# Kernel tuning notes

Hardware: AMD Instinct MI355X
Metric: run time of the kernel (lower is better)

## Reference

```python
import jax, jax.numpy as jnp
import numpy as np
from jax import lax

B, CIN, COUT, K, H, W = 16, 512, 512, 3, 64, 64
STYLE_DIM, BASIS, DIRS = 512, 8, 8


def setup_inputs() -> dict:
    key = jax.random.key(0)
    ks = jax.random.split(key, 8)
    return {
        "x": jax.random.normal(ks[0], (B, CIN, H, W), jnp.float32),
        "style": jax.random.normal(ks[1], (B, STYLE_DIM), jnp.float32),
        "weight": jax.random.normal(ks[2], (1, COUT, CIN, K, K), jnp.float32),
        "mod_w": jax.random.normal(ks[3], (CIN, STYLE_DIM), jnp.float32) * 0.02,
        "mod_b": jnp.ones((CIN,), jnp.float32),
        "basis_vectors": jax.random.normal(ks[4], (BASIS, 1, COUT, CIN, K, K), jnp.float32),
        "shifts_coords": jax.random.normal(ks[5], (DIRS, BASIS), jnp.float32),
        "batch_shifts": jax.random.uniform(ks[6], (B,), jnp.float32),
        "batch_directions": jax.random.randint(ks[7], (B,), 0, DIRS),
    }


def reference(x, style, weight, mod_w, mod_b, basis_vectors, shifts_coords,
              batch_shifts, batch_directions):
    batch, in_ch, h, w = x.shape
    out_ch, k = weight.shape[1], weight.shape[3]
    scale = 1.0 / np.sqrt(in_ch * k * k)  # StyleGAN2 equalized-lr scale

    # --- deformation: per-sample weight delta from basis subspace ---
    coefs = shifts_coords[batch_directions]                     # [B, basis]
    bv = basis_vectors.reshape(basis_vectors.shape[0], -1)      # [basis, O*I*k*k]
    delta = coefs @ bv                                          # [B, P]
    nrm = jnp.linalg.norm(delta, axis=1, keepdims=True)
    delta = delta / jnp.maximum(nrm, 1e-12) * batch_shifts[:, None]
    delta = delta.reshape(batch, out_ch, in_ch, k, k)
    wgt = weight + delta                                        # [B, O, I, k, k]

    # --- style modulation + demodulation ---
    s = style @ mod_w.T + mod_b                                 # [B, I]
    wgt = scale * wgt * s[:, None, :, None, None]
    demod = lax.rsqrt(jnp.sum(wgt * wgt, axis=(2, 3, 4)) + 1e-8)  # [B, O]
    wgt = wgt * demod[:, :, None, None, None]

    # --- grouped conv, groups = batch ---
    wgt = wgt.reshape(batch * out_ch, in_ch, k, k)
    xg = x.reshape(1, batch * in_ch, h, w)
    pad = k // 2
    out = lax.conv_general_dilated(
        xg, wgt, window_strides=(1, 1), padding=[(pad, pad), (pad, pad)],
        feature_group_count=batch,
        dimension_numbers=("NCHW", "OIHW", "NCHW"))
    return out.reshape(batch, out_ch, h, w)
```

## Files before the change

kernel.cpp:

```cpp
#include <hip/hip_runtime.h>


typedef __attribute__((ext_vector_type(8))) short bf16x8;
typedef __attribute__((ext_vector_type(4))) float f32x4;

__device__ __forceinline__ unsigned short f2bf(float f) {
  unsigned u = __float_as_uint(f);
  return (unsigned short)((u + 0x7FFFu + ((u >> 16) & 1u)) >> 16);
}

__device__ __forceinline__ void gl_lds16(const void* g, void* l) {
  __builtin_amdgcn_global_load_lds(
      (const __attribute__((address_space(1))) void*)g,
      (__attribute__((address_space(3))) void*)l, 16, 0, 0);
}

template <int N> __device__ __forceinline__ void vm_wait() {
  if constexpr (N == 8) asm volatile("s_waitcnt vmcnt(8)" ::: "memory");
  else if constexpr (N == 0) asm volatile("s_waitcnt vmcnt(0)" ::: "memory");
}

__global__ __launch_bounds__(256) void k_pad(const float* __restrict__ x,
                                             unsigned short* __restrict__ xp) {
  const int bx = blockIdx.x;
  const int b   = bx >> 9;
  const int rem = bx & 511;
  const int y   = rem >> 3;
  const int cb  = rem & 7;
  const int t = threadIdx.x;
  __shared__ float tile[64][65];
  const float* src = x + ((size_t)(b * 512 + cb * 64) * 4096) + y * 64;
#pragma unroll
  for (int r = 0; r < 4; ++r) {
    int idx = r * 256 + t;
    int ch = idx >> 4;
    int xq = (idx & 15) << 2;
    float4 v = *(const float4*)(src + (size_t)ch * 4096 + xq);
    tile[ch][xq + 0] = v.x; tile[ch][xq + 1] = v.y;
    tile[ch][xq + 2] = v.z; tile[ch][xq + 3] = v.w;
  }
  const uint4 z4 = {0u, 0u, 0u, 0u};
  if (t < 16) {
    const int side = t >> 3;
    const int lo = (t & 7) * 8;
    unsigned short* p =
        xp + (((size_t)(b * 66 + y + 1) * 66 + side * 65) * 512 + cb * 64 + lo);
    *(uint4*)p = z4;
  }
  if (y == 0 || y == 63) {
    const int row = (y == 0) ? 0 : 65;
    for (int idx = t; idx < 528; idx += 256) {
      const int c = idx >> 3;
      const int lo = (idx & 7) * 8;
      unsigned short* p =
          xp + (((size_t)(b * 66 + row) * 66 + c) * 512 + cb * 64 + lo);
      *(uint4*)p = z4;
    }
  }
  __syncthreads();
  const int col = t >> 2;
  const int q = t & 3;
  union { unsigned short u16[16]; uint4 v[2]; } pk;
#pragma unroll
  for (int j = 0; j < 16; ++j) pk.u16[j] = f2bf(tile[q * 16 + j][col]);
  unsigned short* dst =
      xp + (((size_t)(b * 66 + y + 1) * 66 + col + 1) * 512 + cb * 64 + q * 16);
  *(uint4*)dst = pk.v[0];
  *(uint4*)(dst + 8) = pk.v[1];
}

__global__ __launch_bounds__(256) void k_mod(const float* __restrict__ style,
                                             const float* __restrict__ mod_w,
                                             const float* __restrict__ mod_b,
                                             float* __restrict__ smod) {
  const int b = blockIdx.x;
  __shared__ float st[512];
  for (int d = threadIdx.x; d < 512; d += 256) st[d] = style[b * 512 + d];
  __syncthreads();
  for (int i = threadIdx.x; i < 512; i += 256) {
    const float* wr = mod_w + (size_t)i * 512;
    float acc = 0.f;
#pragma unroll 4
    for (int d = 0; d < 512; d += 4) {
      float4 wv = *(const float4*)(wr + d);
      acc += wv.x * st[d] + wv.y * st[d + 1] + wv.z * st[d + 2] + wv.w * st[d + 3];
    }
    smod[b * 512 + i] = acc + mod_b[i];
  }
}

__global__ __launch_bounds__(256, 3) void k_gram(const float* __restrict__ bv,
                                                 float* __restrict__ G) {
  const int P4 = 589824;
  float a[36];
#pragma unroll
  for (int c = 0; c < 36; ++c) a[c] = 0.f;
  const float4* bv4 = (const float4*)bv;
  for (int p = blockIdx.x * 256 + threadIdx.x; p < P4; p += gridDim.x * 256) {
    float4 v[8];
#pragma unroll
    for (int k = 0; k < 8; ++k) v[k] = bv4[(size_t)k * P4 + p];
    int c = 0;
#pragma unroll
    for (int i = 0; i < 8; ++i)
#pragma unroll
      for (int j = i; j < 8; ++j) {
        a[c] += v[i].x * v[j].x + v[i].y * v[j].y + v[i].z * v[j].z +
                v[i].w * v[j].w;
        ++c;
      }
  }
#pragma unroll
  for (int c = 0; c < 36; ++c)
#pragma unroll
    for (int off = 32; off > 0; off >>= 1) a[c] += __shfl_down(a[c], off);
  __shared__ float red[4][36];
  const int wv = threadIdx.x >> 6;
  if ((threadIdx.x & 63) == 0)
#pragma unroll
    for (int c = 0; c < 36; ++c) red[wv][c] = a[c];
  __syncthreads();
  if (threadIdx.x < 36)
    atomicAdd(&G[threadIdx.x], red[0][threadIdx.x] + red[1][threadIdx.x] +
                                   red[2][threadIdx.x] + red[3][threadIdx.x]);
}

__global__ void k_amp(const float* __restrict__ shifts_coords,
                      const float* __restrict__ batch_shifts,
                      const int* __restrict__ dirs, const float* __restrict__ G,
                      float* __restrict__ camp) {
  const int b = threadIdx.x;
  if (b < 16) {
    const int dir = dirs[b];
    float c[8];
    for (int k = 0; k < 8; ++k) c[k] = shifts_coords[dir * 8 + k];
    float n2 = 0.f;
    int idx = 0;
    for (int i = 0; i < 8; ++i)
      for (int j = i; j < 8; ++j) {
        float g = G[idx++];
        n2 += (i == j) ? c[i] * c[i] * g : 2.f * c[i] * c[j] * g;
      }
    float nrm = sqrtf(fmaxf(n2, 0.f));
    float amp = batch_shifts[b] / fmaxf(nrm, 1e-12f);
    for (int k = 0; k < 8; ++k) camp[b * 8 + k] = c[k] * amp;
  }
}

__global__ __launch_bounds__(512) void k_weights(const float* __restrict__ weight,
                                                 const float* __restrict__ bv,
                                                 const float* __restrict__ smod,
                                                 const float* __restrict__ camp,
                                                 unsigned short* __restrict__ wgt,
                                                 float* __restrict__ demod) {
  const int o = blockIdx.x;
  const int i = threadIdx.x;
  __shared__ float cl[128];
  __shared__ float red[8][16];
  if (threadIdx.x < 128) cl[threadIdx.x] = camp[threadIdx.x];
  __syncthreads();
  const float scl = 0.014731391274719738f;
  float sm[16];
#pragma unroll
  for (int b = 0; b < 16; ++b) sm[b] = smod[b * 512 + i] * scl;
  float ssq[16];
#pragma unroll
  for (int b = 0; b < 16; ++b) ssq[b] = 0.f;
  const size_t base = ((size_t)o * 512 + i) * 9;
#pragma unroll
  for (int g = 0; g < 3; ++g) {
    float w[3], v[8][3];
#pragma unroll
    for (int q = 0; q < 3; ++q) w[q] = weight[base + g * 3 + q];
#pragma unroll
    for (int k = 0; k < 8; ++k)
#pragma unroll
      for (int q = 0; q < 3; ++q)
        v[k][q] = bv[(size_t)k * 2359296 + base + g * 3 + q];
#pragma unroll
    for (int b = 0; b < 16; ++b) {
#pragma unroll
      for (int q = 0; q < 3; ++q) {
        float d = w[q];
#pragma unroll
        for (int k = 0; k < 8; ++k) d = fmaf(cl[b * 8 + k], v[k][q], d);
        float wv = d * sm[b];
        ssq[b] = fmaf(wv, wv, ssq[b]);
        wgt[(((size_t)(b * 9 + g * 3 + q) * 512 + o) << 9) + i] = f2bf(wv);
      }
    }
  }
#pragma unroll
  for (int b = 0; b < 16; ++b)
#pragma unroll
    for (int off = 32; off > 0; off >>= 1) ssq[b] += __shfl_down(ssq[b], off);
  const int wv_ = threadIdx.x >> 6;
  if ((threadIdx.x & 63) == 0)
#pragma unroll
    for (int b = 0; b < 16; ++b) red[wv_][b] = ssq[b];
  __syncthreads();
  if (threadIdx.x < 16) {
    float s = 0.f;
#pragma unroll
    for (int wq = 0; wq < 8; ++wq) s += red[wq][threadIdx.x];
    demod[threadIdx.x * 512 + o] = rsqrtf(s + 1e-8f);
  }
}

__global__ __launch_bounds__(512, 2) void k_conv(
    const unsigned short* __restrict__ xp, const unsigned short* __restrict__ wgt,
    const float* __restrict__ demod, float* __restrict__ out) {
  extern __shared__ unsigned char smem[];
  const int tid = threadIdx.x;
  const int l = tid & 63;
  const int w = tid >> 6;
  const int wo = w >> 2;
  const int wn = w & 3;

  const int bid = blockIdx.x;
  const int bz = (bid & 7) * 64 + (bid >> 3);
  const int b = bz >> 5;
  const int tt = bz & 31;
  const int o0 = (tt >> 4) << 8;
  const int tn = tt & 15;
  const int n0 = tn << 8;
  const int y0 = tn << 2;

  int swzS[4];
  size_t aByte[4], pBase[4];
#pragma unroll
  for (int r = 0; r < 4; ++r) {
    const int idx = r * 512 + tid;
    const int row = idx >> 3;
    const int swz = ((idx & 7) << 4) ^ ((row & 7) << 4);
    swzS[r] = swz;
    aByte[r] = ((size_t)(o0 + row) << 10) + swz;
    pBase[r] = (size_t)(b * 66 + y0 + (row >> 6)) * 66 + (row & 63);
  }

  const char* wgtc = (const char*)wgt;
  const char* xpc = (const char*)xp;

  auto stage_all = [&](unsigned char* buf, int kt) {
    const int kk = kt >> 3;
    const int is = kt & 7;
    const int ky = kk / 3;
    const int kx = kk - ky * 3;
    const size_t aPlane = ((size_t)(b * 9 + kk) << 19) + ((size_t)is << 7);
    unsigned char* lA = buf;
    unsigned char* lB = buf + 32768;
#pragma unroll
    for (int r = 0; r < 4; ++r)
      gl_lds16(wgtc + aPlane + aByte[r], lA + (r * 512 + tid) * 16);
#pragma unroll
    for (int r = 0; r < 4; ++r)
      gl_lds16(xpc + (((pBase[r] + ky * 66 + kx) << 10) + ((size_t)is << 7) +
                      swzS[r]),
               lB + (r * 512 + tid) * 16);
  };

  f32x4 acc[8][4];
  const f32x4 zz = {0.f, 0.f, 0.f, 0.f};
#pragma unroll
  for (int mi = 0; mi < 8; ++mi)
#pragma unroll
    for (int ni = 0; ni < 4; ++ni) acc[mi][ni] = zz;
  bf16x8 af0[8], af1[8], bf0[4], bf1[4];

  auto rdA = [&](const unsigned char* lA, int MH, bf16x8 (&afx)[8]) {
#pragma unroll
    for (int mi = 0; mi < 4; ++mi)
#pragma unroll
      for (int ks = 0; ks < 2; ++ks) {
        const int row = MH * 128 + wo * 64 + mi * 16 + (l & 15);
        afx[mi * 2 + ks] = *(const bf16x8*)(
            lA + row * 128 + ((ks * 64 + ((l >> 4) << 4)) ^ ((row & 7) << 4)));
      }
  };
  auto rdB = [&](const unsigned char* lB, int NH, bf16x8 (&bfx)[4]) {
#pragma unroll
    for (int ni = 0; ni < 2; ++ni)
#pragma unroll
      for (int ks = 0; ks < 2; ++ks) {
        const int row = NH * 128 + wn * 32 + ni * 16 + (l & 15);
        bfx[ni * 2 + ks] = *(const bf16x8*)(
            lB + row * 128 + ((ks * 64 + ((l >> 4) << 4)) ^ ((row & 7) << 4)));
      }
  };
  auto mma = [&](int MH, int NH, bf16x8 (&afx)[8], bf16x8 (&bfx)[4]) {
    __builtin_amdgcn_s_setprio(1);
#pragma unroll
    for (int mi = 0; mi < 4; ++mi)
#pragma unroll
      for (int ni = 0; ni < 2; ++ni)
#pragma unroll
        for (int ks = 0; ks < 2; ++ks)
          acc[MH * 4 + mi][NH * 2 + ni] =
              __builtin_amdgcn_mfma_f32_16x16x32_bf16(
                  afx[mi * 2 + ks], bfx[ni * 2 + ks],
                  acc[MH * 4 + mi][NH * 2 + ni], 0, 0, 0);
    __builtin_amdgcn_s_setprio(0);
  };

  stage_all(smem, 0);
  stage_all(smem + 65536, 1);
  vm_wait<8>();
  __builtin_amdgcn_s_barrier();

  int cur = 0;
#pragma unroll 1
  for (int kt = 0; kt < 72; ++kt) {
    unsigned char* lA = smem + (cur << 16);
    unsigned char* lB = lA + 32768;
    rdA(lA, 0, af0);
    rdB(lB, 0, bf0);
    rdB(lB, 1, bf1);
    rdA(lA, 1, af1);
    mma(0, 0, af0, bf0);
    mma(0, 1, af0, bf1);
    asm volatile("s_waitcnt lgkmcnt(0)" ::: "memory");
    __builtin_amdgcn_sched_barrier(0);
    __builtin_amdgcn_s_barrier();
    __builtin_amdgcn_sched_barrier(0);
    if (kt < 70) stage_all(lA, kt + 2);
    mma(1, 1, af1, bf1);
    mma(1, 0, af1, bf0);
    if (kt < 70) {
      vm_wait<8>();
      __builtin_amdgcn_s_barrier();
      __builtin_amdgcn_sched_barrier(0);
    } else if (kt == 70) {
      vm_wait<0>();
      __builtin_amdgcn_s_barrier();
      __builtin_amdgcn_sched_barrier(0);
    }
    cur ^= 1;
  }

  float* outb = out + (size_t)(b * 512 + o0) * 4096 + n0;
#pragma unroll
  for (int mh = 0; mh < 2; ++mh)
#pragma unroll
    for (int mi = 0; mi < 4; ++mi) {
      const int orow = mh * 128 + wo * 64 + mi * 16 + ((l >> 4) << 2);
      float dm[4];
#pragma unroll
      for (int r = 0; r < 4; ++r) dm[r] = demod[b * 512 + o0 + orow + r];
#pragma unroll
      for (int nh = 0; nh < 2; ++nh)
#pragma unroll
        for (int ni = 0; ni < 2; ++ni) {
          const int pix = nh * 128 + wn * 32 + ni * 16 + (l & 15);
#pragma unroll
          for (int r = 0; r < 4; ++r)
            outb[(size_t)(orow + r) * 4096 + pix] =
                acc[mh * 4 + mi][nh * 2 + ni][r] * dm[r];
        }
    }
}

extern "C" void kernel_launch(void* const* d_in, const int* in_sizes, int n_in,
                              void* d_out, int out_size, void* d_ws,
                              size_t ws_size, hipStream_t stream) {
  const float* x      = (const float*)d_in[0];
  const float* style  = (const float*)d_in[1];
  const float* weight = (const float*)d_in[2];
  const float* mod_w  = (const float*)d_in[3];
  const float* mod_b  = (const float*)d_in[4];
  const float* bv     = (const float*)d_in[5];
  const float* sc     = (const float*)d_in[6];
  const float* bsh    = (const float*)d_in[7];
  const int*   bdir   = (const int*)d_in[8];
  float* out = (float*)d_out;

  char* ws = (char*)d_ws;
  unsigned short* xp  = (unsigned short*)(ws);
  unsigned short* wgt = (unsigned short*)(ws + 71368704);
  float* G     = (float*)(ws + 146866176);
  float* camp  = (float*)(ws + 146866432);
  float* smod  = (float*)(ws + 146866944);
  float* demod = (float*)(ws + 146899712);

  hipFuncSetAttribute((const void*)k_conv,
                      hipFuncAttributeMaxDynamicSharedMemorySize, 131072);

  hipMemsetAsync(G, 0, 256, stream);
  k_pad<<<8192, 256, 0, stream>>>(x, xp);
  k_mod<<<16, 256, 0, stream>>>(style, mod_w, mod_b, smod);
  k_gram<<<1024, 256, 0, stream>>>(bv, G);
  k_amp<<<1, 64, 0, stream>>>(sc, bsh, bdir, G, camp);
  k_weights<<<512, 512, 0, stream>>>(weight, bv, smod, camp, wgt, demod);
  k_conv<<<512, 512, 131072, stream>>>(xp, wgt, demod, out);
}
```

Before: 418.2 us.

## Use triple-buffered K=32 pipeline with one barrier per step in conv

The conv GEMM main loop moves from a double-buffered K=64 stage with two barriers per step to a triple-buffered K=32 stage (144 steps) with a single barrier each. Each wave now owns a contiguous 128x64 output tile and issues all 32 MFMAs after loading its fragments once, instead of splitting the work into four half-tile phases. The LDS XOR swizzle is dropped for a plain 64-byte row layout, and occupancy hints and dynamic LDS are resized to match. The aim is less barrier stall and better overlap of global-to-LDS loads with compute, at the cost of more loop iterations and possible LDS bank conflicts from the unswizzled reads.

```diff
diff --git a/kernel.cpp b/kernel.cpp
--- a/kernel.cpp
+++ b/kernel.cpp
@@ -16,7 +16,7 @@
 }
 
 template <int N> __device__ __forceinline__ void vm_wait() {
-  if constexpr (N == 8) asm volatile("s_waitcnt vmcnt(8)" ::: "memory");
+  if constexpr (N == 4) asm volatile("s_waitcnt vmcnt(4)" ::: "memory");
   else if constexpr (N == 0) asm volatile("s_waitcnt vmcnt(0)" ::: "memory");
 }
 
@@ -207,7 +207,7 @@
   }
 }
 
-__global__ __launch_bounds__(512, 2) void k_conv(
+__global__ __launch_bounds__(512, 1) void k_conv(
     const unsigned short* __restrict__ xp, const unsigned short* __restrict__ wgt,
     const float* __restrict__ demod, float* __restrict__ out) {
   extern __shared__ unsigned char smem[];
@@ -226,36 +226,36 @@
   const int n0 = tn << 8;
   const int y0 = tn << 2;
 
-  int swzS[4];
-  size_t aByte[4], pBase[4];
-#pragma unroll
-  for (int r = 0; r < 4; ++r) {
+  size_t aOff[2], pBase[2];
+  int sOff[2];
+#pragma unroll
+  for (int r = 0; r < 2; ++r) {
     const int idx = r * 512 + tid;
-    const int row = idx >> 3;
-    const int swz = ((idx & 7) << 4) ^ ((row & 7) << 4);
-    swzS[r] = swz;
-    aByte[r] = ((size_t)(o0 + row) << 10) + swz;
+    const int row = idx >> 2;
+    const int slot = idx & 3;
+    aOff[r] = ((size_t)(o0 + row) << 10) + slot * 16;
     pBase[r] = (size_t)(b * 66 + y0 + (row >> 6)) * 66 + (row & 63);
+    sOff[r] = slot * 16;
   }
 
   const char* wgtc = (const char*)wgt;
   const char* xpc = (const char*)xp;
 
-  auto stage_all = [&](unsigned char* buf, int kt) {
-    const int kk = kt >> 3;
-    const int is = kt & 7;
+  auto stage = [&](unsigned char* buf, int kt) {
+    const int kk = kt >> 4;
+    const int is = kt & 15;
     const int ky = kk / 3;
     const int kx = kk - ky * 3;
-    const size_t aPlane = ((size_t)(b * 9 + kk) << 19) + ((size_t)is << 7);
+    const size_t aPlane = ((size_t)(b * 9 + kk) << 19) + ((size_t)is << 6);
     unsigned char* lA = buf;
-    unsigned char* lB = buf + 32768;
-#pragma unroll
-    for (int r = 0; r < 4; ++r)
-      gl_lds16(wgtc + aPlane + aByte[r], lA + (r * 512 + tid) * 16);
-#pragma unroll
-    for (int r = 0; r < 4; ++r)
-      gl_lds16(xpc + (((pBase[r] + ky * 66 + kx) << 10) + ((size_t)is << 7) +
-                      swzS[r]),
+    unsigned char* lB = buf + 16384;
+#pragma unroll
+    for (int r = 0; r < 2; ++r)
+      gl_lds16(wgtc + aPlane + aOff[r], lA + (r * 512 + tid) * 16);
+#pragma unroll
+    for (int r = 0; r < 2; ++r)
+      gl_lds16(xpc + (((pBase[r] + ky * 66 + kx) << 10) + ((size_t)is << 6) +
+                      sOff[r]),
                lB + (r * 512 + tid) * 16);
   };
 
@@ -265,98 +265,67 @@
   for (int mi = 0; mi < 8; ++mi)
 #pragma unroll
     for (int ni = 0; ni < 4; ++ni) acc[mi][ni] = zz;
-  bf16x8 af0[8], af1[8], bf0[4], bf1[4];
-
-  auto rdA = [&](const unsigned char* lA, int MH, bf16x8 (&afx)[8]) {
-#pragma unroll
-    for (int mi = 0; mi < 4; ++mi)
-#pragma unroll
-      for (int ks = 0; ks < 2; ++ks) {
-        const int row = MH * 128 + wo * 64 + mi * 16 + (l & 15);
-        afx[mi * 2 + ks] = *(const bf16x8*)(
-            lA + row * 128 + ((ks * 64 + ((l >> 4) << 4)) ^ ((row & 7) << 4)));
-      }
-  };
-  auto rdB = [&](const unsigned char* lB, int NH, bf16x8 (&bfx)[4]) {
-#pragma unroll
-    for (int ni = 0; ni < 2; ++ni)
-#pragma unroll
-      for (int ks = 0; ks < 2; ++ks) {
-        const int row = NH * 128 + wn * 32 + ni * 16 + (l & 15);
-        bfx[ni * 2 + ks] = *(const bf16x8*)(
-            lB + row * 128 + ((ks * 64 + ((l >> 4) << 4)) ^ ((row & 7) << 4)));
-      }
-  };
-  auto mma = [&](int MH, int NH, bf16x8 (&afx)[8], bf16x8 (&bfx)[4]) {
+  bf16x8 af[8], bf[4];
+
+  const int rdoff = (l >> 4) << 4;
+
+  unsigned char* p0 = smem;
+  unsigned char* p1 = smem + 32768;
+  unsigned char* p2 = smem + 65536;
+  stage(p0, 0);
+  stage(p1, 1);
+  vm_wait<4>();
+  __builtin_amdgcn_s_barrier();
+  __builtin_amdgcn_sched_barrier(0);
+
+#pragma unroll 1
+  for (int kt = 0; kt < 144; ++kt) {
+    const unsigned char* lA = p0;
+    const unsigned char* lB = p0 + 16384;
+#pragma unroll
+    for (int ni = 0; ni < 4; ++ni) {
+      const int row = wn * 64 + ni * 16 + (l & 15);
+      bf[ni] = *(const bf16x8*)(lB + row * 64 + rdoff);
+    }
+#pragma unroll
+    for (int mi = 0; mi < 8; ++mi) {
+      const int row = wo * 128 + mi * 16 + (l & 15);
+      af[mi] = *(const bf16x8*)(lA + row * 64 + rdoff);
+    }
+    if (kt <= 141) stage(p2, kt + 2);
     __builtin_amdgcn_s_setprio(1);
 #pragma unroll
-    for (int mi = 0; mi < 4; ++mi)
-#pragma unroll
-      for (int ni = 0; ni < 2; ++ni)
-#pragma unroll
-        for (int ks = 0; ks < 2; ++ks)
-          acc[MH * 4 + mi][NH * 2 + ni] =
-              __builtin_amdgcn_mfma_f32_16x16x32_bf16(
-                  afx[mi * 2 + ks], bfx[ni * 2 + ks],
-                  acc[MH * 4 + mi][NH * 2 + ni], 0, 0, 0);
+    for (int mi = 0; mi < 8; ++mi)
+#pragma unroll
+      for (int ni = 0; ni < 4; ++ni)
+        acc[mi][ni] = __builtin_amdgcn_mfma_f32_16x16x32_bf16(
+            af[mi], bf[ni], acc[mi][ni], 0, 0, 0);
     __builtin_amdgcn_s_setprio(0);
-  };
-
-  stage_all(smem, 0);
-  stage_all(smem + 65536, 1);
-  vm_wait<8>();
-  __builtin_amdgcn_s_barrier();
-
-  int cur = 0;
-#pragma unroll 1
-  for (int kt = 0; kt < 72; ++kt) {
-    unsigned char* lA = smem + (cur << 16);
-    unsigned char* lB = lA + 32768;
-    rdA(lA, 0, af0);
-    rdB(lB, 0, bf0);
-    rdB(lB, 1, bf1);
-    rdA(lA, 1, af1);
-    mma(0, 0, af0, bf0);
-    mma(0, 1, af0, bf1);
-    asm volatile("s_waitcnt lgkmcnt(0)" ::: "memory");
     __builtin_amdgcn_sched_barrier(0);
-    __builtin_amdgcn_s_barrier();
-    __builtin_amdgcn_sched_barrier(0);
-    if (kt < 70) stage_all(lA, kt + 2);
-    mma(1, 1, af1, bf1);
-    mma(1, 0, af1, bf0);
-    if (kt < 70) {
-      vm_wait<8>();
+    if (kt <= 141) vm_wait<4>();
+    else if (kt == 142) vm_wait<0>();
+    if (kt <= 142) {
       __builtin_amdgcn_s_barrier();
       __builtin_amdgcn_sched_barrier(0);
-    } else if (kt == 70) {
-      vm_wait<0>();
-      __builtin_amdgcn_s_barrier();
-      __builtin_amdgcn_sched_barrier(0);
-    }
-    cur ^= 1;
+    }
+    unsigned char* tmp = p0; p0 = p1; p1 = p2; p2 = tmp;
   }
 
   float* outb = out + (size_t)(b * 512 + o0) * 4096 + n0;
 #pragma unroll
-  for (int mh = 0; mh < 2; ++mh)
-#pragma unroll
-    for (int mi = 0; mi < 4; ++mi) {
-      const int orow = mh * 128 + wo * 64 + mi * 16 + ((l >> 4) << 2);
-      float dm[4];
-#pragma unroll
-      for (int r = 0; r < 4; ++r) dm[r] = demod[b * 512 + o0 + orow + r];
-#pragma unroll
-      for (int nh = 0; nh < 2; ++nh)
-#pragma unroll
-        for (int ni = 0; ni < 2; ++ni) {
-          const int pix = nh * 128 + wn * 32 + ni * 16 + (l & 15);
-#pragma unroll
-          for (int r = 0; r < 4; ++r)
-            outb[(size_t)(orow + r) * 4096 + pix] =
-                acc[mh * 4 + mi][nh * 2 + ni][r] * dm[r];
-        }
-    }
+  for (int mi = 0; mi < 8; ++mi) {
+    const int orow = wo * 128 + mi * 16 + ((l >> 4) << 2);
+    float dm[4];
+#pragma unroll
+    for (int r = 0; r < 4; ++r) dm[r] = demod[b * 512 + o0 + orow + r];
+#pragma unroll
+    for (int ni = 0; ni < 4; ++ni) {
+      const int pix = wn * 64 + ni * 16 + (l & 15);
+#pragma unroll
+      for (int r = 0; r < 4; ++r)
+        outb[(size_t)(orow + r) * 4096 + pix] = acc[mi][ni][r] * dm[r];
+    }
+  }
 }
 
 extern "C" void kernel_launch(void* const* d_in, const int* in_sizes, int n_in,
@@ -382,7 +351,7 @@
   float* demod = (float*)(ws + 146899712);
 
   hipFuncSetAttribute((const void*)k_conv,
-                      hipFuncAttributeMaxDynamicSharedMemorySize, 131072);
+                      hipFuncAttributeMaxDynamicSharedMemorySize, 98304);
 
   hipMemsetAsync(G, 0, 256, stream);
   k_pad<<<8192, 256, 0, stream>>>(x, xp);
@@ -390,5 +359,5 @@
   k_gram<<<1024, 256, 0, stream>>>(bv, G);
   k_amp<<<1, 64, 0, stream>>>(sc, bsh, bdir, G, camp);
   k_weights<<<512, 512, 0, stream>>>(weight, bv, smod, camp, wgt, demod);
-  k_conv<<<512, 512, 131072, stream>>>(xp, wgt, demod, out);
-}
+  k_conv<<<512, 512, 98304, stream>>>(xp, wgt, demod, out);
+}
```

After: 437.0 us. +4.5%, slower.

## Split tile staging into quarter loads interleaved with MFMA phases

Applied to the files above, without the earlier changes.

The prefetch of the next K-tile is broken into four quarter-stages (two for the weight tile, two for the input tile), and each is issued between the MFMA sub-blocks with barriers and partial vmcnt waits. Prefetch depth drops from two tiles ahead to one tile ahead into the alternate buffer. The aim is to spread global-to-LDS traffic across the iteration and overlap it more finely with matrix math. In exchange each iteration now has many more workgroup barriers, and the shallower prefetch gives memory latency less time to hide.

```diff
diff --git a/kernel.cpp b/kernel.cpp
--- a/kernel.cpp
+++ b/kernel.cpp
@@ -16,7 +16,8 @@
 }
 
 template <int N> __device__ __forceinline__ void vm_wait() {
-  if constexpr (N == 8) asm volatile("s_waitcnt vmcnt(8)" ::: "memory");
+  if constexpr (N == 4) asm volatile("s_waitcnt vmcnt(4)" ::: "memory");
+  else if constexpr (N == 2) asm volatile("s_waitcnt vmcnt(2)" ::: "memory");
   else if constexpr (N == 0) asm volatile("s_waitcnt vmcnt(0)" ::: "memory");
 }
 
@@ -241,22 +242,27 @@
   const char* wgtc = (const char*)wgt;
   const char* xpc = (const char*)xp;
 
-  auto stage_all = [&](unsigned char* buf, int kt) {
+  auto stage_half = [&](unsigned char* buf, int kt, int which) {
     const int kk = kt >> 3;
     const int is = kt & 7;
     const int ky = kk / 3;
     const int kx = kk - ky * 3;
-    const size_t aPlane = ((size_t)(b * 9 + kk) << 19) + ((size_t)is << 7);
     unsigned char* lA = buf;
     unsigned char* lB = buf + 32768;
-#pragma unroll
-    for (int r = 0; r < 4; ++r)
-      gl_lds16(wgtc + aPlane + aByte[r], lA + (r * 512 + tid) * 16);
-#pragma unroll
-    for (int r = 0; r < 4; ++r)
-      gl_lds16(xpc + (((pBase[r] + ky * 66 + kx) << 10) + ((size_t)is << 7) +
-                      swzS[r]),
-               lB + (r * 512 + tid) * 16);
+    if (which == 0 || which == 3) {
+      const size_t aPlane = ((size_t)(b * 9 + kk) << 19) + ((size_t)is << 7);
+      const int r0 = (which == 0) ? 0 : 2;
+#pragma unroll
+      for (int r = r0; r < r0 + 2; ++r)
+        gl_lds16(wgtc + aPlane + aByte[r], lA + (r * 512 + tid) * 16);
+    } else {
+      const int r0 = (which == 1) ? 0 : 2;
+#pragma unroll
+      for (int r = r0; r < r0 + 2; ++r)
+        gl_lds16(xpc + (((pBase[r] + ky * 66 + kx) << 10) + ((size_t)is << 7) +
+                        swzS[r]),
+                 lB + (r * 512 + tid) * 16);
+    }
   };
 
   f32x4 acc[8][4];
@@ -300,40 +306,57 @@
                   afx[mi * 2 + ks], bfx[ni * 2 + ks],
                   acc[MH * 4 + mi][NH * 2 + ni], 0, 0, 0);
     __builtin_amdgcn_s_setprio(0);
+    __builtin_amdgcn_sched_barrier(0);
   };
 
-  stage_all(smem, 0);
-  stage_all(smem + 65536, 1);
-  vm_wait<8>();
+  stage_half(smem, 0, 0);
+  stage_half(smem, 0, 1);
+  stage_half(smem, 0, 2);
+  stage_half(smem, 0, 3);
+  vm_wait<4>();
   __builtin_amdgcn_s_barrier();
+  __builtin_amdgcn_sched_barrier(0);
 
   int cur = 0;
 #pragma unroll 1
   for (int kt = 0; kt < 72; ++kt) {
     unsigned char* lA = smem + (cur << 16);
     unsigned char* lB = lA + 32768;
+    unsigned char* nbuf = smem + ((cur ^ 1) << 16);
+    const bool stg = (kt < 71);
     rdA(lA, 0, af0);
     rdB(lB, 0, bf0);
+    if (stg) stage_half(nbuf, kt + 1, 0);
+    __builtin_amdgcn_s_barrier();
+    asm volatile("s_waitcnt lgkmcnt(0)" ::: "memory");
+    __builtin_amdgcn_sched_barrier(0);
+    mma(0, 0, af0, bf0);
+    if (stg) vm_wait<4>(); else vm_wait<2>();
+    __builtin_amdgcn_s_barrier();
+    __builtin_amdgcn_sched_barrier(0);
     rdB(lB, 1, bf1);
+    if (stg) stage_half(nbuf, kt + 1, 1);
+    __builtin_amdgcn_s_barrier();
+    asm volatile("s_waitcnt lgkmcnt(0)" ::: "memory");
+    __builtin_amdgcn_sched_barrier(0);
+    mma(0, 1, af0, bf1);
+    if (stg) vm_wait<4>(); else vm_wait<0>();
+    __builtin_amdgcn_s_barrier();
+    __builtin_amdgcn_sched_barrier(0);
     rdA(lA, 1, af1);
-    mma(0, 0, af0, bf0);
-    mma(0, 1, af0, bf1);
+    if (stg) stage_half(nbuf, kt + 1, 2);
+    __builtin_amdgcn_s_barrier();
     asm volatile("s_waitcnt lgkmcnt(0)" ::: "memory");
     __builtin_amdgcn_sched_barrier(0);
-    __builtin_amdgcn_s_barrier();
-    __builtin_amdgcn_sched_barrier(0);
-    if (kt < 70) stage_all(lA, kt + 2);
     mma(1, 1, af1, bf1);
+    __builtin_amdgcn_s_barrier();
+    __builtin_amdgcn_sched_barrier(0);
+    if (stg) stage_half(nbuf, kt + 1, 3);
+    __builtin_amdgcn_s_barrier();
     mma(1, 0, af1, bf0);
-    if (kt < 70) {
-      vm_wait<8>();
-      __builtin_amdgcn_s_barrier();
-      __builtin_amdgcn_sched_barrier(0);
-    } else if (kt == 70) {
-      vm_wait<0>();
-      __builtin_amdgcn_s_barrier();
-      __builtin_amdgcn_sched_barrier(0);
-    }
+    if (stg) vm_wait<4>();
+    __builtin_amdgcn_s_barrier();
+    __builtin_amdgcn_sched_barrier(0);
     cur ^= 1;
   }
 
```

After: 440.1 us. +5.2%, slower.
